# Kernel tuning notes

Measured on AMD Instinct MI355X. Metric: run time of the kernel, lower is better.

## Reference

```python
import jax, jax.numpy as jnp
import numpy as np
from jax import lax

B, H, W = 1, 128, 128
KS = 3
N = KS * KS  # 9 deformable sampling points
BN_EPS = 1e-5


def conv2d(x, w, padding=0, stride=1):
    return lax.conv_general_dilated(x, w, (stride, stride),
                                    [(padding, padding), (padding, padding)],
                                    dimension_numbers=('NCHW', 'OIHW', 'NCHW'))


def bn_eval(x, gamma, beta, mean, var):
    scale = gamma / jnp.sqrt(var + BN_EPS)
    return x * scale[None, :, None, None] + (beta - mean * scale)[None, :, None, None]


def upsample_bilinear_ac(x, oh, ow):
    # F.interpolate(mode='bilinear', align_corners=True), separable gather
    b, c, h, w = x.shape
    ys = jnp.linspace(0.0, h - 1.0, oh)
    xs = jnp.linspace(0.0, w - 1.0, ow)
    y0 = jnp.floor(ys).astype(jnp.int32)
    y1 = jnp.minimum(y0 + 1, h - 1)
    wy = (ys - y0).astype(x.dtype)[None, None, :, None]
    x0 = jnp.floor(xs).astype(jnp.int32)
    x1 = jnp.minimum(x0 + 1, w - 1)
    wx = (xs - x0).astype(x.dtype)
    r = x[:, :, y0, :] * (1.0 - wy) + x[:, :, y1, :] * wy
    return r[:, :, :, x0] * (1.0 - wx) + r[:, :, :, x1] * wx


def deform_conv(x, p_w, p_b, dc_w, pad=1):
    # DeformConv2d(inc, outc, ks=3, padding=1, modulation=False):
    # offsets from a 3x3 conv, bilinear gather at p0 + p_n + offset on the
    # zero-padded input, then 3x3 kernel contraction over the 9 samples.
    b, c, h, w = x.shape
    off = conv2d(x, p_w, padding=1) + p_b[None, :, None, None]  # (b, 2N, h, w)
    rng = jnp.arange(KS, dtype=x.dtype) - (KS - 1) // 2          # [-1, 0, 1]
    pnx, pny = jnp.meshgrid(rng, rng, indexing='ij')
    # absolute sampling coords in padded frame, (b, h, w, N)
    px = jnp.transpose(off[:, :N], (0, 2, 3, 1)) + pnx.ravel() + jnp.arange(1, h + 1, dtype=x.dtype)[None, :, None, None]
    py = jnp.transpose(off[:, N:], (0, 2, 3, 1)) + pny.ravel() + jnp.arange(1, w + 1, dtype=x.dtype)[None, None, :, None]
    Hp, Wp = h + 2 * pad, w + 2 * pad
    xp = jnp.pad(x, ((0, 0), (0, 0), (pad, pad), (pad, pad))).reshape(b, c, Hp * Wp)
    fx = jnp.floor(px)
    fy = jnp.floor(py)
    x0f = jnp.clip(fx, 0, Hp - 1)
    x1f = jnp.clip(fx + 1.0, 0, Hp - 1)
    y0f = jnp.clip(fy, 0, Wp - 1)
    y1f = jnp.clip(fy + 1.0, 0, Wp - 1)
    pxc = jnp.clip(px, 0, Hp - 1)
    pyc = jnp.clip(py, 0, Wp - 1)

    def gather(qxf, qyf):
        idx = (qxf.astype(jnp.int32) * Wp + qyf.astype(jnp.int32)).reshape(b, 1, h * w * N)
        g = jnp.take_along_axis(xp, jnp.broadcast_to(idx, (b, c, h * w * N)), axis=2)
        return g.reshape(b, c, h, w, N)

    g_lt = (1.0 + (x0f - pxc)) * (1.0 + (y0f - pyc))
    g_rb = (1.0 - (x1f - pxc)) * (1.0 - (y1f - pyc))
    g_lb = (1.0 + (x0f - pxc)) * (1.0 - (y1f - pyc))
    g_rt = (1.0 - (x1f - pxc)) * (1.0 + (y0f - pyc))
    x_off = (g_lt[:, None] * gather(x0f, y0f) + g_rb[:, None] * gather(x1f, y1f)
             + g_lb[:, None] * gather(x0f, y1f) + g_rt[:, None] * gather(x1f, y0f))
    # conv(kernel=3, stride=3) on the rearranged samples == contraction over N
    return jnp.einsum('bchwk,ock->bohw', x_off, dc_w.reshape(dc_w.shape[0], c, N))


def _forward(x, low_level_feat, fm_w, fs_w, p_w, p_b, dc_w,
             lc1_w, bn1_gamma, bn1_beta, bn1_mean, bn1_var,
             lc2_w, bn2_gamma, bn2_beta, bn2_mean, bn2_var):
    xu = upsample_bilinear_ac(x, H, W)                       # (B,256,128,128)
    Z = low_level_feat                                       # AdaptiveAvgPool2d((128,128)) is identity on 128x128 input
    v = jax.nn.sigmoid(jnp.einsum('oc,bchw->bohw', fm_w, Z))
    u = jnp.einsum('bchk,bckw->bchw', low_level_feat, v) + low_level_feat
    Cf = jnp.einsum('oc,bchw->bohw', fs_w, u)
    cc = jnp.concatenate([xu, Cf], axis=1)                   # (B,512,128,128)
    fam = deform_conv(cc, p_w, p_b, dc_w) + Cf
    up1 = jax.nn.relu(bn_eval(conv2d(fam, lc1_w, padding=1), bn1_gamma, bn1_beta, bn1_mean, bn1_var))
    up2 = jax.nn.relu(bn_eval(conv2d(up1, lc2_w, padding=1), bn2_gamma, bn2_beta, bn2_mean, bn2_var))
    return up1, up2


def setup_inputs():
    key = jax.random.key(0)
    ks = jax.random.split(key, 12)
    f32 = jnp.float32
    return {
        'x': jax.random.normal(ks[0], (B, 256, 32, 32), f32),
        'low_level_feat': jax.random.normal(ks[1], (B, 256, H, W), f32),
        'fm_w': jax.random.normal(ks[2], (256, 256), f32) * 0.0625,
        'fs_w': jax.random.normal(ks[3], (256, 256), f32) * 0.0625,
        'p_w': jax.random.normal(ks[4], (2 * N, 512, 3, 3), f32) * 0.01,
        'p_b': jnp.zeros((2 * N,), f32),
        'dc_w': jax.random.normal(ks[5], (256, 512, 3, 3), f32) * 0.02,
        'lc1_w': jax.random.normal(ks[6], (256, 256, 3, 3), f32) * 0.02,
        'bn1_gamma': jnp.ones((256,), f32),
        'bn1_beta': jnp.zeros((256,), f32),
        'bn1_mean': jax.random.normal(ks[7], (256,), f32) * 0.1,
        'bn1_var': jax.random.uniform(ks[8], (256,), f32) + 0.5,
        'lc2_w': jax.random.normal(ks[9], (256, 256, 3, 3), f32) * 0.02,
        'bn2_gamma': jnp.ones((256,), f32),
        'bn2_beta': jnp.zeros((256,), f32),
        'bn2_mean': jax.random.normal(ks[10], (256,), f32) * 0.1,
        'bn2_var': jax.random.uniform(ks[11], (256,), f32) + 0.5,
    }


def reference(x, low_level_feat, fm_w, fs_w, p_w, p_b, dc_w,
              lc1_w, bn1_gamma, bn1_beta, bn1_mean, bn1_var,
              lc2_w, bn2_gamma, bn2_beta, bn2_mean, bn2_var):
    return _forward(x, low_level_feat, fm_w, fs_w, p_w, p_b, dc_w,
                    lc1_w, bn1_gamma, bn1_beta, bn1_mean, bn1_var,
                    lc2_w, bn2_gamma, bn2_beta, bn2_mean, bn2_var)
```

## Files before the change

kernel.cpp:

```cpp
#include <hip/hip_runtime.h>
#include <math.h>

#define HW   16384
#define PS   16900

typedef __attribute__((ext_vector_type(8))) short bf16x8;
typedef __attribute__((ext_vector_type(4))) float f32x4;

__device__ inline unsigned short f2bf(float x) {
    unsigned int u = __float_as_uint(x);
    unsigned int r = (u + 0x7fffu + ((u >> 16) & 1u)) >> 16;
    return (unsigned short)r;
}
__device__ inline float bf2f(unsigned short h) {
    return __uint_as_float(((unsigned int)h) << 16);
}

__global__ __launch_bounds__(256) void zero_ringP_k(unsigned short* __restrict__ base) {
    int t = blockIdx.x * 256 + threadIdx.x;
    if (t >= 520 * 32) return;
    int ck = (t & 31) << 3, rp = t >> 5;
    int row, col;
    if (rp < 130)      { row = 0;   col = rp; }
    else if (rp < 260) { row = 129; col = rp - 130; }
    else {
        int rem = rp - 260;
        if (rem >= 256) return;
        row = 1 + (rem >> 1); col = (rem & 1) ? 129 : 0;
    }
    bf16x8 z = (bf16x8){0, 0, 0, 0, 0, 0, 0, 0};
    *(bf16x8*)(base + (size_t)(row * 130 + col) * 256 + ck) = z;
}

__global__ __launch_bounds__(256) void ringT_k(unsigned short* __restrict__ ccT) {
    int t = blockIdx.x * 256 + threadIdx.x;
    if (t >= 520 * 256) return;
    int ci = t & 255, rp = t >> 8;
    int row, col;
    if (rp < 130)      { row = 0;   col = rp; }
    else if (rp < 260) { row = 129; col = rp - 130; }
    else {
        int rem = rp - 260;
        if (rem >= 256) return;
        row = 1 + (rem >> 1); col = (rem & 1) ? 129 : 0;
    }
    ccT[(size_t)(row * 130 + col) * 512 + 256 + ci] = 0;
}

__global__ __launch_bounds__(256) void upsample_k(const float* __restrict__ x,
                                                  float* __restrict__ ccpad) {
    int c = blockIdx.y;
    int idx = blockIdx.x * 256 + threadIdx.x;
    if (idx >= PS) return;
    int r = idx / 130, s = idx - r * 130;
    float val = 0.0f;
    if (r >= 1 && r <= 128 && s >= 1 && s <= 128) {
        int i = r - 1, j = s - 1;
        float yf = (float)i * (31.0f / 127.0f);
        float xf = (float)j * (31.0f / 127.0f);
        int y0 = min((int)yf, 31); int y1 = min(y0 + 1, 31);
        int x0 = min((int)xf, 31); int x1 = min(x0 + 1, 31);
        float wy = yf - (float)y0, wx = xf - (float)x0;
        const float* xc = x + (size_t)c * 1024;
        float a = xc[y0 * 32 + x0] * (1.0f - wx) + xc[y0 * 32 + x1] * wx;
        float b = xc[y1 * 32 + x0] * (1.0f - wx) + xc[y1 * 32 + x1] * wx;
        val = a * (1.0f - wy) + b * wy;
    }
    ccpad[(size_t)c * PS + idx] = val;
}

__global__ __launch_bounds__(256) void cvtT_flat_k(const float* __restrict__ src,
                                                   unsigned short* __restrict__ dst,
                                                   int npx) {
    int t = blockIdx.x * 256 + threadIdx.x;
    int c = t & 255, pix = t >> 8;
    dst[t] = f2bf(src[(size_t)c * npx + pix]);
}

__global__ __launch_bounds__(256) void cvtT_k(const float* __restrict__ src,
                                              unsigned short* __restrict__ dst) {
    int t = blockIdx.x * 256 + threadIdx.x;
    int c = t & 255, pix = t >> 8;
    dst[(size_t)pix * 512 + c] = f2bf(src[(size_t)c * PS + pix]);
}

__global__ __launch_bounds__(256) void w2bf_k(const float* __restrict__ a,
                                              const float* __restrict__ b,
                                              unsigned short* __restrict__ da,
                                              unsigned short* __restrict__ db) {
    int t = blockIdx.x * 256 + threadIdx.x;
    if (t >= 65536) return;
    da[t] = f2bf(a[t]);
    db[t] = f2bf(b[t]);
}

__global__ __launch_bounds__(256) void u_matmul_k(const float* __restrict__ llf,
                                                  const float* __restrict__ v,
                                                  float* __restrict__ u) {
    int c = blockIdx.y;
    const float* L = llf + (size_t)c * HW;
    const float* V = v   + (size_t)c * HW;
    float*       U = u   + (size_t)c * HW;
    int tid = threadIdx.x;
    int ty = tid >> 4, tx = tid & 15;
    int r0 = (blockIdx.x << 6) + (ty << 2);
    int w0 = tx << 3;
    float acc[4][8] = {};
    for (int k = 0; k < 128; ++k) {
        float a[4];
#pragma unroll
        for (int i = 0; i < 4; ++i) a[i] = L[(r0 + i) * 128 + k];
        float4 b0 = *(const float4*)(V + k * 128 + w0);
        float4 b1 = *(const float4*)(V + k * 128 + w0 + 4);
        float bv[8] = {b0.x, b0.y, b0.z, b0.w, b1.x, b1.y, b1.z, b1.w};
#pragma unroll
        for (int i = 0; i < 4; ++i)
#pragma unroll
            for (int j = 0; j < 8; ++j) acc[i][j] += a[i] * bv[j];
    }
#pragma unroll
    for (int i = 0; i < 4; ++i) {
#pragma unroll
        for (int j = 0; j < 8; ++j) acc[i][j] += L[(r0 + i) * 128 + w0 + j];
        *(float4*)(U + (r0 + i) * 128 + w0)     = make_float4(acc[i][0], acc[i][1], acc[i][2], acc[i][3]);
        *(float4*)(U + (r0 + i) * 128 + w0 + 4) = make_float4(acc[i][4], acc[i][5], acc[i][6], acc[i][7]);
    }
}

__global__ __launch_bounds__(256) void tr_dcwF9_k(const float* __restrict__ w,
                                                  unsigned short* __restrict__ dst) {
    int t = blockIdx.x * 256 + threadIdx.x;
    if (t >= 1179648) return;
    int e    = t & 7;
    int lane = (t >> 3) & 63;
    int f    = t >> 9;
    int mi   = f & 1;
    int s    = (f >> 1) & 1;
    int wv   = (f >> 2) & 7;
    int ch   = f >> 5;
    int kt   = ch >> 3;
    int o = (wv << 5) + (mi << 4) + (lane & 15);
    int c = ((ch & 7) << 6) + (s << 5) + ((lane >> 4) << 3) + e;
    dst[t] = f2bf(w[(size_t)o * 4608 + c * 9 + kt]);
}

__global__ __launch_bounds__(256) void tr_lcF_k(const float* __restrict__ w,
                                                unsigned short* __restrict__ dst) {
    int t = blockIdx.x * 256 + threadIdx.x;
    if (t >= 589824) return;
    int e    = t & 7;
    int lane = (t >> 3) & 63;
    int mi   = (t >> 9) & 3;
    int kss  = (t >> 11) & 7;
    int wo   = (t >> 14) & 3;
    int kt   = t >> 16;
    int o = (wo << 6) + (mi << 4) + (lane & 15);
    int c = (kss << 5) + ((lane >> 4) << 3) + e;
    dst[t] = f2bf(w[(size_t)o * 2304 + c * 9 + kt]);
}

__global__ __launch_bounds__(256) void tr_pw_k(const float* __restrict__ w,
                                               unsigned short* __restrict__ dst) {
    int t = blockIdx.x * 256 + threadIdx.x;
    if (t >= 9 * 32 * 512) return;
    int c = t & 511; int rest = t >> 9; int o = rest & 31; int k = rest >> 5;
    dst[t] = (o < 18) ? f2bf(w[(size_t)o * 4608 + c * 9 + k]) : (unsigned short)0;
}

__global__ __launch_bounds__(256, 2) void vmfma_k(
        const unsigned short* __restrict__ inT,
        const unsigned short* __restrict__ wh,
        float* __restrict__ vout) {
    __shared__ __align__(16) unsigned short Bs[32][72];
    int b = blockIdx.x;
    int xcd = b & 7, sl = b >> 3;
    int nt = (xcd << 6) + sl;
    int hrow = nt >> 2, pc0 = (nt & 3) << 5;
    int tid = threadIdx.x;
    int wv = tid >> 6, lane = tid & 63;
    int lr = lane & 15, lg = lane >> 4;
    int pxs = tid >> 3, cg8 = tid & 7;
    int p = (hrow << 7) + pc0 + pxs;
    f32x4 acc[4][2];
#pragma unroll
    for (int i = 0; i < 4; ++i)
#pragma unroll
        for (int j = 0; j < 2; ++j) acc[i][j] = (f32x4){0.f, 0.f, 0.f, 0.f};
    for (int ks = 0; ks < 256; ks += 64) {
        __syncthreads();
        *(bf16x8*)&Bs[pxs][cg8 << 3] =
            *(const bf16x8*)(inT + (size_t)p * 256 + ks + (cg8 << 3));
        __syncthreads();
#pragma unroll
        for (int s = 0; s < 2; ++s) {
            int ko = ks + (s << 5) + (lg << 3);
            bf16x8 af[4], bfr[2];
#pragma unroll
            for (int mi = 0; mi < 4; ++mi)
                af[mi] = *(const bf16x8*)(wh + (size_t)((wv << 6) + (mi << 4) + lr) * 256 + ko);
#pragma unroll
            for (int ni = 0; ni < 2; ++ni)
                bfr[ni] = *(const bf16x8*)(&Bs[(ni << 4) + lr][(s << 5) + (lg << 3)]);
#pragma unroll
            for (int mi = 0; mi < 4; ++mi)
#pragma unroll
                for (int ni = 0; ni < 2; ++ni)
                    acc[mi][ni] = __builtin_amdgcn_mfma_f32_16x16x32_bf16(
                        af[mi], bfr[ni], acc[mi][ni], 0, 0, 0);
        }
    }
#pragma unroll
    for (int mi = 0; mi < 4; ++mi)
#pragma unroll
        for (int ni = 0; ni < 2; ++ni)
#pragma unroll
            for (int r = 0; r < 4; ++r) {
                int o   = (wv << 6) + (mi << 4) + (lg << 2) + r;
                int pxx = pc0 + (ni << 4) + lr;
                vout[(size_t)o * HW + (hrow << 7) + pxx] =
                    1.0f / (1.0f + expf(-acc[mi][ni][r]));
            }
}

__global__ __launch_bounds__(256, 2) void cfmfma_k(
        const unsigned short* __restrict__ inT,
        const unsigned short* __restrict__ wh,
        unsigned short* __restrict__ ccT) {
    __shared__ __align__(16) unsigned short Bs[32][72];
    int b = blockIdx.x;
    int xcd = b & 7, sl = b >> 3;
    int nt = (xcd << 6) + sl;
    int hrow = nt >> 2, pc0 = (nt & 3) << 5;
    int tid = threadIdx.x;
    int wv = tid >> 6, lane = tid & 63;
    int lr = lane & 15, lg = lane >> 4;
    int pxs = tid >> 3, cg8 = tid & 7;
    int p = (hrow << 7) + pc0 + pxs;
    f32x4 acc[4][2];
#pragma unroll
    for (int i = 0; i < 4; ++i)
#pragma unroll
        for (int j = 0; j < 2; ++j) acc[i][j] = (f32x4){0.f, 0.f, 0.f, 0.f};
    for (int ks = 0; ks < 256; ks += 64) {
        __syncthreads();
        *(bf16x8*)&Bs[pxs][cg8 << 3] =
            *(const bf16x8*)(inT + (size_t)p * 256 + ks + (cg8 << 3));
        __syncthreads();
#pragma unroll
        for (int s = 0; s < 2; ++s) {
            int ko = ks + (s << 5) + (lg << 3);
            bf16x8 af[4], bfr[2];
#pragma unroll
            for (int mi = 0; mi < 4; ++mi)
                af[mi] = *(const bf16x8*)(wh + (size_t)((wv << 6) + (mi << 4) + lr) * 256 + ko);
#pragma unroll
            for (int ni = 0; ni < 2; ++ni)
                bfr[ni] = *(const bf16x8*)(&Bs[(ni << 4) + lr][(s << 5) + (lg << 3)]);
#pragma unroll
            for (int mi = 0; mi < 4; ++mi)
#pragma unroll
                for (int ni = 0; ni < 2; ++ni)
                    acc[mi][ni] = __builtin_amdgcn_mfma_f32_16x16x32_bf16(
                        af[mi], bfr[ni], acc[mi][ni], 0, 0, 0);
        }
    }
#pragma unroll
    for (int mi = 0; mi < 4; ++mi)
#pragma unroll
        for (int ni = 0; ni < 2; ++ni) {
            int pxx = pc0 + (ni << 4) + lr;
            int pix = (hrow + 1) * 130 + pxx + 1;
            unsigned short pk[4];
#pragma unroll
            for (int r = 0; r < 4; ++r) pk[r] = f2bf(acc[mi][ni][r]);
            *(ushort4*)(ccT + (size_t)pix * 512 + 256 + (wv << 6) + (mi << 4) + (lg << 2))
                = *(ushort4*)pk;
        }
}

__global__ __launch_bounds__(256, 2) void off_part_k(
        const unsigned short* __restrict__ ccT,
        const unsigned short* __restrict__ pwTh,
        float* __restrict__ pbuf) {
    __shared__ __align__(16) unsigned short Bs[128][40];
    int b = blockIdx.x;
    int xcd = b & 7, slot = b >> 3;
    int hrow = (xcd << 4) + (slot >> 2);
    int cg = slot & 3, c0 = cg << 7;
    int tid = threadIdx.x;
    int wv = tid >> 6, lane = tid & 63;
    int wr = wv >> 1, wc = wv & 1;
    int lr = lane & 15, lg = lane >> 4;
    int c4 = tid & 3, pxs = tid >> 2;
    f32x4 acc[4];
#pragma unroll
    for (int j = 0; j < 4; ++j) acc[j] = (f32x4){0.f, 0.f, 0.f, 0.f};

    for (int kt = 0; kt < 9; ++kt) {
        int dy = kt / 3 - 1, dx = kt % 3 - 1;
        int pixb = (hrow + dy + 1) * 130 + dx + 1;
        for (int ksl = 0; ksl < 128; ksl += 32) {
            __syncthreads();
#pragma unroll
            for (int pp = 0; pp < 2; ++pp) {
                int px = pxs + (pp << 6);
                *(bf16x8*)&Bs[px][c4 << 3] =
                    *(const bf16x8*)(ccT + (size_t)(pixb + px) * 512 + c0 + ksl + (c4 << 3));
            }
            __syncthreads();
            bf16x8 af, bfr[4];
            af = *(const bf16x8*)(pwTh + (size_t)kt * 16384
                                  + (size_t)((wr << 4) + lr) * 512 + c0 + ksl + (lg << 3));
#pragma unroll
            for (int ni = 0; ni < 4; ++ni) {
                int n = (wc << 6) + (ni << 4) + lr;
                bfr[ni] = *(const bf16x8*)(&Bs[n][lg << 3]);
            }
#pragma unroll
            for (int ni = 0; ni < 4; ++ni)
                acc[ni] = __builtin_amdgcn_mfma_f32_16x16x32_bf16(af, bfr[ni], acc[ni], 0, 0, 0);
        }
    }
#pragma unroll
    for (int ni = 0; ni < 4; ++ni)
#pragma unroll
        for (int r = 0; r < 4; ++r) {
            int o = (wr << 4) + (lg << 2) + r;
            int p = (hrow << 7) + (wc << 6) + (ni << 4) + lr;
            pbuf[(size_t)((cg << 5) + o) * HW + p] = acc[ni][r];
        }
}

__global__ __launch_bounds__(256) void make_idx_k(const float* __restrict__ pbuf,
                                                  const float* __restrict__ pb,
                                                  int4* __restrict__ IDX,
                                                  float4* __restrict__ WT) {
    int t = blockIdx.x * 256 + threadIdx.x;
    if (t >= 9 * HW) return;
    int k = t >> 14, p = t & 16383;
    int h = p >> 7, w = p & 127;
    float ox = 0.f, oy = 0.f;
#pragma unroll
    for (int cg = 0; cg < 4; ++cg) {
        ox += pbuf[(size_t)((cg << 5) + k) * HW + p];
        oy += pbuf[(size_t)((cg << 5) + 9 + k) * HW + p];
    }
    float px = ox + pb[k]     + (float)(k / 3 - 1) + (float)(h + 1);
    float py = oy + pb[9 + k] + (float)(k % 3 - 1) + (float)(w + 1);
    float fx = floorf(px), fy = floorf(py);
    float x0 = fminf(fmaxf(fx,        0.f), 129.f);
    float x1 = fminf(fmaxf(fx + 1.0f, 0.f), 129.f);
    float y0 = fminf(fmaxf(fy,        0.f), 129.f);
    float y1 = fminf(fmaxf(fy + 1.0f, 0.f), 129.f);
    float pxc = fminf(fmaxf(px, 0.f), 129.f);
    float pyc = fminf(fmaxf(py, 0.f), 129.f);
    float gx0 = 1.0f + x0 - pxc, gx1 = 1.0f - x1 + pxc;
    float gy0 = 1.0f + y0 - pyc, gy1 = 1.0f - y1 + pyc;
    int ix0 = (int)x0, ix1 = (int)x1, iy0 = (int)y0, iy1 = (int)y1;
    IDX[t] = make_int4((ix0 * 130 + iy0) << 9, (ix1 * 130 + iy1) << 9,
                       (ix0 * 130 + iy1) << 9, (ix1 * 130 + iy0) << 9);
    WT[t]  = make_float4(gx0 * gy0, gx1 * gy1, gx0 * gy1, gx1 * gy0);
}

__global__ __launch_bounds__(512, 4) void fam9_k(
        const unsigned short* __restrict__ ccT,
        const unsigned short* __restrict__ dcwF,
        const int4* __restrict__ IDX, const float4* __restrict__ WT,
        unsigned short* __restrict__ part0,
        unsigned short* __restrict__ part1) {
    __shared__ __align__(16) unsigned short Bs[2][64][72];
    int b = blockIdx.x;
    int khalf = b >> 8;
    int bb = b & 255;
    int xcd = bb & 7, sl = bb >> 3;
    int nt = (xcd << 5) + sl;
    int hrow = nt >> 1, pc0 = (nt & 1) << 6;
    int tid = threadIdx.x;
    int wv = tid >> 6, lane = tid & 63;
    int lr = lane & 15, lg = lane >> 4;
    int pxg = tid >> 3, grp = tid & 7;
    int p2 = (hrow << 7) + pc0 + pxg;
    const unsigned short* wfb = dcwF + ((size_t)wv << 11) + ((size_t)lane << 3);
    f32x4 acc[2][4];
#pragma unroll
    for (int i = 0; i < 2; ++i)
#pragma unroll
        for (int j = 0; j < 4; ++j) acc[i][j] = (f32x4){0.f, 0.f, 0.f, 0.f};

    bf16x8 v0, v1, v2, v3;
    bf16x8 Aa00, Aa01, Aa10, Aa11;
    bf16x8 Ba00, Ba01, Ba10, Ba11;

#define ISSUE_A9(S, ch) do {                                                  \
    const unsigned short* ap_ = wfb + ((size_t)(ch) << 14);                   \
    S##00 = *(const bf16x8*)(ap_);                                            \
    S##01 = *(const bf16x8*)(ap_ + 512);                                      \
    S##10 = *(const bf16x8*)(ap_ + 1024);                                     \
    S##11 = *(const bf16x8*)(ap_ + 1536);                                     \
} while (0)

#define ISSUE_G9(ch, idm) do {                                                \
    int cb_ = (((ch) & 7) << 6) + (grp << 3);                                 \
    v0 = *(const bf16x8*)(ccT + (idm).x + cb_);                               \
    v1 = *(const bf16x8*)(ccT + (idm).y + cb_);                               \
    v2 = *(const bf16x8*)(ccT + (idm).z + cb_);                               \
    v3 = *(const bf16x8*)(ccT + (idm).w + cb_);                               \
} while (0)

#define NEXT_G9(cn) do {                                                      \
    if ((cn) < c1) {                                                          \
        if (((cn) & 7) == 0) {                                                \
            idc = idn; wtc = wtn;                                             \
            int kt2_ = ((cn) >> 3) + 1;                                       \
            if ((kt2_ << 3) < c1) {                                           \
                idn = IDX[(kt2_ << 14) + p2];                                 \
                wtn = WT [(kt2_ << 14) + p2];                                 \
            }                                                                 \
        }                                                                     \
        ISSUE_G9(cn, idc);                                                    \
        wnext = wtc;                                                          \
    }                                                                         \
} while (0)

#define PUBLISH9(bi) do {                                                     \
    unsigned short pk_[8];                                                    \
    _Pragma("unroll")                                                         \
    for (int e_ = 0; e_ < 8; ++e_) {                                          \
        float val_ = wcur.x * bf2f((unsigned short)v0[e_])                    \
                   + wcur.y * bf2f((unsigned short)v1[e_])                    \
                   + wcur.z * bf2f((unsigned short)v2[e_])                    \
                   + wcur.w * bf2f((unsigned short)v3[e_]);                   \
        pk_[e_] = f2bf(val_);                                                 \
    }                                                                         \
    *(bf16x8*)&Bs[bi][pxg][grp << 3] = *(bf16x8*)pk_;                         \
} while (0)

#define MFMA9(S, bi) do {                                                     \
    _Pragma("unroll")                                                         \
    for (int ni_ = 0; ni_ < 4; ++ni_) {                                       \
        bf16x8 b0_ = *(const bf16x8*)(&Bs[bi][(ni_ << 4) + lr][lg << 3]);     \
        acc[0][ni_] = __builtin_amdgcn_mfma_f32_16x16x32_bf16(S##00, b0_, acc[0][ni_], 0, 0, 0); \
        acc[1][ni_] = __builtin_amdgcn_mfma_f32_16x16x32_bf16(S##01, b0_, acc[1][ni_], 0, 0, 0); \
    }                                                                         \
    _Pragma("unroll")                                                         \
    for (int ni_ = 0; ni_ < 4; ++ni_) {                                       \
        bf16x8 b1_ = *(const bf16x8*)(&Bs[bi][(ni_ << 4) + lr][32 + (lg << 3)]); \
        acc[0][ni_] = __builtin_amdgcn_mfma_f32_16x16x32_bf16(S##10, b1_, acc[0][ni_], 0, 0, 0); \
        acc[1][ni_] = __builtin_amdgcn_mfma_f32_16x16x32_bf16(S##11, b1_, acc[1][ni_], 0, 0, 0); \
    }                                                                         \
} while (0)

    int c0 = khalf * 36, c1 = c0 + 36;
    int kt0 = c0 >> 3;
    int4   idc = IDX[(kt0 << 14) + p2];
    float4 wtc = WT [(kt0 << 14) + p2];
    int4   idn = IDX[((kt0 + 1) << 14) + p2];
    float4 wtn = WT [((kt0 + 1) << 14) + p2];
    ISSUE_G9(c0, idc);
    float4 wcur = wtc, wnext = wtc;
    ISSUE_A9(Aa, c0);

    for (int c = c0; c < c1; c += 2) {
        PUBLISH9(0);
        NEXT_G9(c + 1);
        ISSUE_A9(Ba, c + 1);
        __syncthreads();
        MFMA9(Aa, 0);
        wcur = wnext;
        PUBLISH9(1);
        NEXT_G9(c + 2);
        if (c + 2 < c1) ISSUE_A9(Aa, c + 2);
        __syncthreads();
        MFMA9(Ba, 1);
        wcur = wnext;
    }
#undef ISSUE_A9
#undef ISSUE_G9
#undef NEXT_G9
#undef PUBLISH9
#undef MFMA9

    unsigned short* pt = khalf ? part1 : part0;
#pragma unroll
    for (int mi = 0; mi < 2; ++mi)
#pragma unroll
        for (int ni = 0; ni < 4; ++ni) {
            int pxx = pc0 + (ni << 4) + lr;
            int p = (hrow << 7) + pxx;
            unsigned short pk[4];
#pragma unroll
            for (int r = 0; r < 4; ++r) pk[r] = f2bf(acc[mi][ni][r]);
            *(ushort4*)(pt + (size_t)p * 256 + (wv << 5) + (mi << 4) + (lg << 2))
                = *(ushort4*)pk;
        }
}

__global__ __launch_bounds__(256) void combineT_k(
        const unsigned short* __restrict__ p0,
        const unsigned short* __restrict__ p1,
        const unsigned short* __restrict__ ccT,
        unsigned short* __restrict__ famT) {
    int t = blockIdx.x * 256 + threadIdx.x;
    int o8 = (t & 31) << 3, p = t >> 5;
    int row = p >> 7, col = p & 127;
    int pix = (row + 1) * 130 + col + 1;
    bf16x8 a = *(const bf16x8*)(p0 + (size_t)p * 256 + o8);
    bf16x8 b = *(const bf16x8*)(p1 + (size_t)p * 256 + o8);
    bf16x8 c = *(const bf16x8*)(ccT + (size_t)pix * 512 + 256 + o8);
    unsigned short out[8];
#pragma unroll
    for (int e = 0; e < 8; ++e)
        out[e] = f2bf(bf2f((unsigned short)a[e]) + bf2f((unsigned short)b[e])
                      + bf2f((unsigned short)c[e]));
    *(bf16x8*)(famT + (size_t)pix * 256 + o8) = *(bf16x8*)out;
}

__global__ __launch_bounds__(256, 2) void conv2T_k(
        const unsigned short* __restrict__ inT,
        const unsigned short* __restrict__ wF,
        const float* __restrict__ gam, const float* __restrict__ bet,
        const float* __restrict__ mean, const float* __restrict__ var,
        float* __restrict__ out_flat,
        unsigned short* __restrict__ out_padT) {
    __shared__ __align__(16) unsigned short Ls[102][264];
    __shared__ float scs[256], bis[256];
    int b = blockIdx.x;
    int xcd = b & 7, slot = b >> 3;
    int nt = (xcd << 6) + slot;
    int hrow = nt >> 2, pc0 = (nt & 3) << 5;
    int tid = threadIdx.x;
    int wv = tid >> 6, lane = tid & 63;
    int lr = lane & 15, lg = lane >> 4;
    {
        float sc = gam[tid] * rsqrtf(var[tid] + 1e-5f);
        scs[tid] = sc;
        bis[tid] = bet[tid] - mean[tid] * sc;
    }
#pragma unroll
    for (int r = 0; r < 3; ++r) {
        const unsigned short* src = inT + (size_t)((hrow + r) * 130 + pc0) * 256;
#pragma unroll
        for (int ps = 0; ps < 5; ++ps) {
            int idx = ps * 2048 + tid * 8;
            if (idx < 8704) {
                bf16x8 v = *(const bf16x8*)(src + idx);
                *(bf16x8*)&Ls[r * 34 + (idx >> 8)][idx & 255] = v;
            }
        }
    }
    __syncthreads();

    f32x4 acc[4][2];
#pragma unroll
    for (int i = 0; i < 4; ++i)
#pragma unroll
        for (int j = 0; j < 2; ++j) acc[i][j] = (f32x4){0.f, 0.f, 0.f, 0.f};

    const unsigned short* wvb = wF + ((size_t)wv << 14) + ((size_t)lane << 3);
    for (int kt = 0; kt < 9; ++kt) {
        int rowb = (kt / 3) * 34 + (kt % 3);
        const unsigned short* wkb = wvb + (size_t)kt * 65536;
#pragma unroll
        for (int kss = 0; kss < 8; ++kss) {
            int ks = kss << 5;
            bf16x8 af[4], bfr[2];
#pragma unroll
            for (int mi = 0; mi < 4; ++mi)
                af[mi] = *(const bf16x8*)(wkb + (size_t)kss * 2048 + mi * 512);
#pragma unroll
            for (int ni = 0; ni < 2; ++ni)
                bfr[ni] = *(const bf16x8*)(&Ls[rowb + (ni << 4) + lr][ks + (lg << 3)]);
#pragma unroll
            for (int mi = 0; mi < 4; ++mi)
#pragma unroll
                for (int ni = 0; ni < 2; ++ni)
                    acc[mi][ni] = __builtin_amdgcn_mfma_f32_16x16x32_bf16(
                        af[mi], bfr[ni], acc[mi][ni], 0, 0, 0);
        }
    }

#pragma unroll
    for (int mi = 0; mi < 4; ++mi)
#pragma unroll
        for (int ni = 0; ni < 2; ++ni) {
            int pxx = pc0 + (ni << 4) + lr;
            unsigned short pk[4];
#pragma unroll
            for (int r = 0; r < 4; ++r) {
                int o = (wv << 6) + (mi << 4) + (lg << 2) + r;
                float rv = fmaxf(acc[mi][ni][r] * scs[o] + bis[o], 0.0f);
                out_flat[(size_t)o * HW + (hrow << 7) + pxx] = rv;
                pk[r] = f2bf(rv);
            }
            if (out_padT) {
                int pix = (hrow + 1) * 130 + pxx + 1;
                *(ushort4*)(out_padT + (size_t)pix * 256 + (wv << 6) + (mi << 4) + (lg << 2))
                    = *(ushort4*)pk;
            }
        }
}

extern "C" void kernel_launch(void* const* d_in, const int* in_sizes, int n_in,
                              void* d_out, int out_size, void* d_ws, size_t ws_size,
                              hipStream_t stream) {
    const float* x     = (const float*)d_in[0];
    const float* llf   = (const float*)d_in[1];
    const float* fm_w  = (const float*)d_in[2];
    const float* fs_w  = (const float*)d_in[3];
    const float* p_w   = (const float*)d_in[4];
    const float* p_b   = (const float*)d_in[5];
    const float* dc_w  = (const float*)d_in[6];
    const float* lc1_w = (const float*)d_in[7];
    const float* bn1g  = (const float*)d_in[8];
    const float* bn1b  = (const float*)d_in[9];
    const float* bn1m  = (const float*)d_in[10];
    const float* bn1v  = (const float*)d_in[11];
    const float* lc2_w = (const float*)d_in[12];
    const float* bn2g  = (const float*)d_in[13];
    const float* bn2b  = (const float*)d_in[14];
    const float* bn2m  = (const float*)d_in[15];
    const float* bn2v  = (const float*)d_in[16];
    float* out1 = (float*)d_out;
    float* out2 = out1 + (size_t)256 * HW;

    if (ws_size < 79839232u) return;
    char* ws = (char*)d_ws;
    unsigned short* ccT   = (unsigned short*)ws;
    float*          ccpad = (float*)(ws + 17305600);
    float*          vbuf  = (float*)(ws + 17305600);
    unsigned short* famT  = (unsigned short*)(ws + 17305600);
    unsigned short* up1T  = (unsigned short*)(ws + 26091520);
    unsigned short* llfT  = (unsigned short*)(ws + 34877440);
    unsigned short* uT    = (unsigned short*)(ws + 43266048);
    unsigned short* part0 = (unsigned short*)(ws + 43266048);
    unsigned short* fmwh  = (unsigned short*)(ws + 51654656);
    unsigned short* fswh  = (unsigned short*)(ws + 51785728);
    float*          ubuf  = (float*)(ws + 51916800);
    float*          pbuf  = (float*)(ws + 51916800);
    unsigned short* part1 = (unsigned short*)(ws + 51916800);
    int4*           IDX   = (int4*)  (ws + 60305408);
    float4*         WT    = (float4*)(ws + 62664704);
    unsigned short* dcwF   = (unsigned short*)(ws + 68694016);
    unsigned short* lcw1F  = (unsigned short*)(ws + 71053312);
    unsigned short* lcw2F  = (unsigned short*)(ws + 72232960);
    unsigned short* pwTh   = (unsigned short*)(ws + 73412608);

    upsample_k<<<dim3(67, 256), 256, 0, stream>>>(x, ccpad);
    cvtT_k<<<dim3(16900), 256, 0, stream>>>(ccpad, ccT);
    cvtT_flat_k<<<dim3(16384), 256, 0, stream>>>(llf, llfT, HW);
    w2bf_k<<<dim3(256), 256, 0, stream>>>(fm_w, fs_w, fmwh, fswh);
    vmfma_k<<<dim3(512), 256, 0, stream>>>(llfT, fmwh, vbuf);
    u_matmul_k<<<dim3(2, 256), 256, 0, stream>>>(llf, vbuf, ubuf);
    cvtT_flat_k<<<dim3(16384), 256, 0, stream>>>(ubuf, uT, HW);
    tr_dcwF9_k<<<dim3(4608), 256, 0, stream>>>(dc_w, dcwF);
    tr_lcF_k<<<dim3(2304), 256, 0, stream>>>(lc1_w, lcw1F);
    tr_lcF_k<<<dim3(2304), 256, 0, stream>>>(lc2_w, lcw2F);
    tr_pw_k<<<dim3(576), 256, 0, stream>>>(p_w, pwTh);
    cfmfma_k<<<dim3(512), 256, 0, stream>>>(uT, fswh, ccT);
    ringT_k<<<dim3(520), 256, 0, stream>>>(ccT);
    off_part_k<<<dim3(512), 256, 0, stream>>>(ccT, pwTh, pbuf);
    make_idx_k<<<dim3(576), 256, 0, stream>>>(pbuf, p_b, IDX, WT);
    zero_ringP_k<<<dim3(65), 256, 0, stream>>>(famT);
    zero_ringP_k<<<dim3(65), 256, 0, stream>>>(up1T);
    fam9_k<<<dim3(512), 512, 0, stream>>>(ccT, dcwF, IDX, WT, part0, part1);
    combineT_k<<<dim3(2048), 256, 0, stream>>>(part0, part1, ccT, famT);
    conv2T_k<<<dim3(512), 256, 0, stream>>>(famT, lcw1F, bn1g, bn1b, bn1m, bn1v,
                                            out1, up1T);
    conv2T_k<<<dim3(512), 256, 0, stream>>>(up1T, lcw2F, bn2g, bn2b, bn2m, bn2v,
                                            out2, nullptr);
}
```

Measured before the change: 451.0 us.

## Split deformable conv reduction three ways and XOR-swizzle LDS tile

The deformable-conv MFMA kernel now splits the 72 reduction chunks into three slices of 24 instead of two of 36. This launches 768 blocks rather than 512, and the launch-bounds hint for blocks per CU rises from 4 to 6. The LDS B tile is written and read with an XOR swizzle on the 8-element group index to reduce bank conflicts. The combine kernel now sums three bf16 partials, adding extra partial-buffer traffic. A third partial buffer reuses the llfT workspace region, which must no longer be live at this point.

```diff
diff --git a/kernel.cpp b/kernel.cpp
--- a/kernel.cpp
+++ b/kernel.cpp
@@ -362,15 +362,16 @@
     WT[t]  = make_float4(gx0 * gy0, gx1 * gy1, gx0 * gy1, gx1 * gy0);
 }
 
-__global__ __launch_bounds__(512, 4) void fam9_k(
+__global__ __launch_bounds__(512, 6) void fam10_k(
         const unsigned short* __restrict__ ccT,
         const unsigned short* __restrict__ dcwF,
         const int4* __restrict__ IDX, const float4* __restrict__ WT,
         unsigned short* __restrict__ part0,
-        unsigned short* __restrict__ part1) {
+        unsigned short* __restrict__ part1,
+        unsigned short* __restrict__ part2) {
     __shared__ __align__(16) unsigned short Bs[2][64][72];
     int b = blockIdx.x;
-    int khalf = b >> 8;
+    int kq = b >> 8;
     int bb = b & 255;
     int xcd = bb & 7, sl = bb >> 3;
     int nt = (xcd << 5) + sl;
@@ -380,6 +381,8 @@
     int lr = lane & 15, lg = lane >> 4;
     int pxg = tid >> 3, grp = tid & 7;
     int p2 = (hrow << 7) + pc0 + pxg;
+    int wgrp = grp ^ (pxg & 7);
+    int rsw = lr & 7;
     const unsigned short* wfb = dcwF + ((size_t)wv << 11) + ((size_t)lane << 3);
     f32x4 acc[2][4];
 #pragma unroll
@@ -432,25 +435,25 @@
                    + wcur.w * bf2f((unsigned short)v3[e_]);                   \
         pk_[e_] = f2bf(val_);                                                 \
     }                                                                         \
-    *(bf16x8*)&Bs[bi][pxg][grp << 3] = *(bf16x8*)pk_;                         \
+    *(bf16x8*)&Bs[bi][pxg][wgrp << 3] = *(bf16x8*)pk_;                        \
 } while (0)
 
 #define MFMA9(S, bi) do {                                                     \
     _Pragma("unroll")                                                         \
     for (int ni_ = 0; ni_ < 4; ++ni_) {                                       \
-        bf16x8 b0_ = *(const bf16x8*)(&Bs[bi][(ni_ << 4) + lr][lg << 3]);     \
+        bf16x8 b0_ = *(const bf16x8*)(&Bs[bi][(ni_ << 4) + lr][(lg ^ rsw) << 3]); \
         acc[0][ni_] = __builtin_amdgcn_mfma_f32_16x16x32_bf16(S##00, b0_, acc[0][ni_], 0, 0, 0); \
         acc[1][ni_] = __builtin_amdgcn_mfma_f32_16x16x32_bf16(S##01, b0_, acc[1][ni_], 0, 0, 0); \
     }                                                                         \
     _Pragma("unroll")                                                         \
     for (int ni_ = 0; ni_ < 4; ++ni_) {                                       \
-        bf16x8 b1_ = *(const bf16x8*)(&Bs[bi][(ni_ << 4) + lr][32 + (lg << 3)]); \
+        bf16x8 b1_ = *(const bf16x8*)(&Bs[bi][(ni_ << 4) + lr][((4 + lg) ^ rsw) << 3]); \
         acc[0][ni_] = __builtin_amdgcn_mfma_f32_16x16x32_bf16(S##10, b1_, acc[0][ni_], 0, 0, 0); \
         acc[1][ni_] = __builtin_amdgcn_mfma_f32_16x16x32_bf16(S##11, b1_, acc[1][ni_], 0, 0, 0); \
     }                                                                         \
 } while (0)
 
-    int c0 = khalf * 36, c1 = c0 + 36;
+    int c0 = kq * 24, c1 = c0 + 24;
     int kt0 = c0 >> 3;
     int4   idc = IDX[(kt0 << 14) + p2];
     float4 wtc = WT [(kt0 << 14) + p2];
@@ -480,7 +483,7 @@
 #undef PUBLISH9
 #undef MFMA9
 
-    unsigned short* pt = khalf ? part1 : part0;
+    unsigned short* pt = (kq == 0) ? part0 : (kq == 1) ? part1 : part2;
 #pragma unroll
     for (int mi = 0; mi < 2; ++mi)
 #pragma unroll
@@ -495,9 +498,10 @@
         }
 }
 
-__global__ __launch_bounds__(256) void combineT_k(
+__global__ __launch_bounds__(256) void combine3_k(
         const unsigned short* __restrict__ p0,
         const unsigned short* __restrict__ p1,
+        const unsigned short* __restrict__ p2,
         const unsigned short* __restrict__ ccT,
         unsigned short* __restrict__ famT) {
     int t = blockIdx.x * 256 + threadIdx.x;
@@ -506,12 +510,13 @@
     int pix = (row + 1) * 130 + col + 1;
     bf16x8 a = *(const bf16x8*)(p0 + (size_t)p * 256 + o8);
     bf16x8 b = *(const bf16x8*)(p1 + (size_t)p * 256 + o8);
+    bf16x8 d = *(const bf16x8*)(p2 + (size_t)p * 256 + o8);
     bf16x8 c = *(const bf16x8*)(ccT + (size_t)pix * 512 + 256 + o8);
     unsigned short out[8];
 #pragma unroll
     for (int e = 0; e < 8; ++e)
         out[e] = f2bf(bf2f((unsigned short)a[e]) + bf2f((unsigned short)b[e])
-                      + bf2f((unsigned short)c[e]));
+                      + bf2f((unsigned short)d[e]) + bf2f((unsigned short)c[e]));
     *(bf16x8*)(famT + (size_t)pix * 256 + o8) = *(bf16x8*)out;
 }
 
@@ -631,6 +636,7 @@
     unsigned short* famT  = (unsigned short*)(ws + 17305600);
     unsigned short* up1T  = (unsigned short*)(ws + 26091520);
     unsigned short* llfT  = (unsigned short*)(ws + 34877440);
+    unsigned short* part2 = (unsigned short*)(ws + 34877440);
     unsigned short* uT    = (unsigned short*)(ws + 43266048);
     unsigned short* part0 = (unsigned short*)(ws + 43266048);
     unsigned short* fmwh  = (unsigned short*)(ws + 51654656);
@@ -662,8 +668,8 @@
     make_idx_k<<<dim3(576), 256, 0, stream>>>(pbuf, p_b, IDX, WT);
     zero_ringP_k<<<dim3(65), 256, 0, stream>>>(famT);
     zero_ringP_k<<<dim3(65), 256, 0, stream>>>(up1T);
-    fam9_k<<<dim3(512), 512, 0, stream>>>(ccT, dcwF, IDX, WT, part0, part1);
-    combineT_k<<<dim3(2048), 256, 0, stream>>>(part0, part1, ccT, famT);
+    fam10_k<<<dim3(768), 512, 0, stream>>>(ccT, dcwF, IDX, WT, part0, part1, part2);
+    combine3_k<<<dim3(2048), 256, 0, stream>>>(part0, part1, part2, ccT, famT);
     conv2T_k<<<dim3(512), 256, 0, stream>>>(famT, lcw1F, bn1g, bn1b, bn1m, bn1v,
                                             out1, up1T);
     conv2T_k<<<dim3(512), 256, 0, stream>>>(up1T, lcw2F, bn2g, bn2b, bn2m, bn2v,
```

Result: slower. 745.3 us (+65.3%).

## Stage 3-row halo tile in LDS once for offset conv instead of per-tap reloads

Applied to the files above, without the earlier changes.

The offset-conv kernel now loads a 3-row x 66-pixel x 128-channel halo tile into LDS once, with a single barrier. All 9 taps read from that tile instead of reloading global data with two barriers per 32-channel slice. The grid doubles by splitting each row into two 64-pixel halves, so each wave holds only two accumulators. This removes repeated global loads and syncs, at the cost of about 52KB of LDS per block, which may limit occupancy.

```diff
diff --git a/kernel.cpp b/kernel.cpp
--- a/kernel.cpp
+++ b/kernel.cpp
@@ -278,56 +278,57 @@
         }
 }
 
-__global__ __launch_bounds__(256, 2) void off_part_k(
+__global__ __launch_bounds__(256, 2) void off_part2_k(
         const unsigned short* __restrict__ ccT,
         const unsigned short* __restrict__ pwTh,
         float* __restrict__ pbuf) {
-    __shared__ __align__(16) unsigned short Bs[128][40];
+    __shared__ __align__(16) unsigned short Ls[198][132];
     int b = blockIdx.x;
     int xcd = b & 7, slot = b >> 3;
-    int hrow = (xcd << 4) + (slot >> 2);
-    int cg = slot & 3, c0 = cg << 7;
+    int hrow = (xcd << 4) + (slot >> 3);
+    int rest = slot & 7;
+    int pxh = rest >> 2, cg = rest & 3;
+    int pc0h = pxh << 6, c0 = cg << 7;
     int tid = threadIdx.x;
     int wv = tid >> 6, lane = tid & 63;
-    int wr = wv >> 1, wc = wv & 1;
     int lr = lane & 15, lg = lane >> 4;
-    int c4 = tid & 3, pxs = tid >> 2;
-    f32x4 acc[4];
-#pragma unroll
-    for (int j = 0; j < 4; ++j) acc[j] = (f32x4){0.f, 0.f, 0.f, 0.f};
-
+    int wo = wv & 1;
+    int pt0 = (wv >> 1) << 1;
+    int chk = tid & 15, pxi0 = tid >> 4;
+#pragma unroll
+    for (int r = 0; r < 3; ++r) {
+        const unsigned short* src = ccT + (size_t)((hrow + r) * 130 + pc0h) * 512 + c0;
+        for (int pxi = pxi0; pxi < 66; pxi += 16)
+            *(bf16x8*)&Ls[r * 66 + pxi][chk << 3] =
+                *(const bf16x8*)(src + (size_t)pxi * 512 + (chk << 3));
+    }
+    __syncthreads();
+
+    f32x4 acc[2];
+    acc[0] = (f32x4){0.f, 0.f, 0.f, 0.f};
+    acc[1] = (f32x4){0.f, 0.f, 0.f, 0.f};
     for (int kt = 0; kt < 9; ++kt) {
-        int dy = kt / 3 - 1, dx = kt % 3 - 1;
-        int pixb = (hrow + dy + 1) * 130 + dx + 1;
-        for (int ksl = 0; ksl < 128; ksl += 32) {
-            __syncthreads();
-#pragma unroll
-            for (int pp = 0; pp < 2; ++pp) {
-                int px = pxs + (pp << 6);
-                *(bf16x8*)&Bs[px][c4 << 3] =
-                    *(const bf16x8*)(ccT + (size_t)(pixb + px) * 512 + c0 + ksl + (c4 << 3));
+        int rowb = (kt / 3) * 66 + (kt % 3);
+        const unsigned short* wk = pwTh + (size_t)kt * 16384
+                                 + (size_t)((wo << 4) + lr) * 512 + c0;
+#pragma unroll
+        for (int ks = 0; ks < 128; ks += 32) {
+            bf16x8 af = *(const bf16x8*)(wk + ks + (lg << 3));
+#pragma unroll
+            for (int pi = 0; pi < 2; ++pi) {
+                int px = ((pt0 + pi) << 4) + lr;
+                bf16x8 bfr = *(const bf16x8*)(&Ls[rowb + px][ks + (lg << 3)]);
+                acc[pi] = __builtin_amdgcn_mfma_f32_16x16x32_bf16(af, bfr, acc[pi], 0, 0, 0);
             }
-            __syncthreads();
-            bf16x8 af, bfr[4];
-            af = *(const bf16x8*)(pwTh + (size_t)kt * 16384
-                                  + (size_t)((wr << 4) + lr) * 512 + c0 + ksl + (lg << 3));
-#pragma unroll
-            for (int ni = 0; ni < 4; ++ni) {
-                int n = (wc << 6) + (ni << 4) + lr;
-                bfr[ni] = *(const bf16x8*)(&Bs[n][lg << 3]);
-            }
-#pragma unroll
-            for (int ni = 0; ni < 4; ++ni)
-                acc[ni] = __builtin_amdgcn_mfma_f32_16x16x32_bf16(af, bfr[ni], acc[ni], 0, 0, 0);
-        }
-    }
-#pragma unroll
-    for (int ni = 0; ni < 4; ++ni)
+        }
+    }
+#pragma unroll
+    for (int pi = 0; pi < 2; ++pi)
 #pragma unroll
         for (int r = 0; r < 4; ++r) {
-            int o = (wr << 4) + (lg << 2) + r;
-            int p = (hrow << 7) + (wc << 6) + (ni << 4) + lr;
-            pbuf[(size_t)((cg << 5) + o) * HW + p] = acc[ni][r];
+            int o = (wo << 4) + (lg << 2) + r;
+            int p = (hrow << 7) + pc0h + ((pt0 + pi) << 4) + lr;
+            pbuf[(size_t)((cg << 5) + o) * HW + p] = acc[pi][r];
         }
 }
 
@@ -658,7 +659,7 @@
     tr_pw_k<<<dim3(576), 256, 0, stream>>>(p_w, pwTh);
     cfmfma_k<<<dim3(512), 256, 0, stream>>>(uT, fswh, ccT);
     ringT_k<<<dim3(520), 256, 0, stream>>>(ccT);
-    off_part_k<<<dim3(512), 256, 0, stream>>>(ccT, pwTh, pbuf);
+    off_part2_k<<<dim3(1024), 256, 0, stream>>>(ccT, pwTh, pbuf);
     make_idx_k<<<dim3(576), 256, 0, stream>>>(pbuf, p_b, IDX, WT);
     zero_ringP_k<<<dim3(65), 256, 0, stream>>>(famT);
     zero_ringP_k<<<dim3(65), 256, 0, stream>>>(up1T);
```

After: 456.5 us. Within noise of the previous version (+1.2%).
